# Optimization experiments

Measured on AMD Instinct MI355X. Metric: run time of the kernel, lower is better.

The kernel has to match this reference:

```python
import jax, jax.numpy as jnp
import numpy as np

B, S, D = 8, 1024, 1024
H, K = 16, 64  # num_heads, key_dim
NEG_INF = -1e9  # Keras _large_compatible_negative for float32


def setup_inputs() -> dict:
    key = jax.random.key(0)
    ks = jax.random.split(key, 10)
    x = jax.random.normal(ks[0], (B, S, D), dtype=jnp.float32)
    mask = jax.random.bernoulli(ks[1], 0.9, (B, S))  # bool per-token mask
    w = lambda k, shp: (0.02 * jax.random.normal(k, shp, dtype=jnp.float32))
    return {
        "input_tensor": x,
        "input_mask": mask,
        "Wq": w(ks[2], (D, H, K)), "bq": jnp.zeros((H, K), jnp.float32),
        "Wk": w(ks[3], (D, H, K)), "bk": jnp.zeros((H, K), jnp.float32),
        "Wv": w(ks[4], (D, H, K)), "bv": jnp.zeros((H, K), jnp.float32),
        "Wo": w(ks[5], (H, K, D)), "bo": jnp.zeros((D,), jnp.float32),
    }


def reference(input_tensor, input_mask, Wq, bq, Wk, bk, Wv, bv, Wo, bo):
    x = input_tensor
    # QKV projections: [B,S,D] x [D,H,K] -> [B,S,H,K]
    q = jnp.einsum("bsd,dhk->bshk", x, Wq) + bq
    k = jnp.einsum("bsd,dhk->bshk", x, Wk) + bk
    v = jnp.einsum("bsd,dhk->bshk", x, Wv) + bv
    # scaled dot-product scores: [B,H,Sq,Sk]
    scores = jnp.einsum("bqhk,bshk->bhqs", q, k) / jnp.sqrt(
        jnp.asarray(K, x.dtype))
    # mask = logical_and(mask[...,None], mask[...,None,:]) per example
    m2 = (input_mask[:, :, None] & input_mask[:, None, :])  # [B,Sq,Sk]
    scores = scores + (1.0 - m2[:, None, :, :].astype(x.dtype)) * NEG_INF
    probs = jax.nn.softmax(scores, axis=-1)
    # attend and project out: [B,S,H,K] -> [B,S,D]
    ctx = jnp.einsum("bhqs,bshk->bqhk", probs, v)
    return jnp.einsum("bqhk,hkd->bqd", ctx, Wo) + bo
```

## Files before the change

kernel.cpp:

```cpp
#include <hip/hip_runtime.h>
#include <math.h>

#define Ss 1024
#define Dd 1024
#define Hh 16
#define Kk 64

typedef __bf16 bf16x8 __attribute__((ext_vector_type(8)));
typedef __bf16 bf16x4 __attribute__((ext_vector_type(4)));
typedef float  f32x4  __attribute__((ext_vector_type(4)));

#define MFMA16(a, b, c) __builtin_amdgcn_mfma_f32_16x16x32_bf16(a, b, c, 0, 0, 0)

#define XB_E   8388608u
#define WT_E   3145728u
#define WOT_E  1048576u
#define QKV_E  8388608u

__global__ __launch_bounds__(256) void prep(
    const float* __restrict__ x,
    const float* __restrict__ Wq, const float* __restrict__ Wk,
    const float* __restrict__ Wv, const float* __restrict__ Wo,
    __bf16* __restrict__ xb, __bf16* __restrict__ WT, __bf16* __restrict__ WoT)
{
    __shared__ float tile[64][65];
    const int z = blockIdx.z;
    const int t = threadIdx.x;

    if (z == 4) {
        size_t blk = blockIdx.y * 16 + blockIdx.x;
        const float4* src = (const float4*)(x + blk * 32768);
        bf16x4* dst = (bf16x4*)(((__bf16*)xb) + blk * 32768);
        #pragma unroll
        for (int u = 0; u < 32; ++u) {
            float4 v = src[u * 256 + t];
            dst[u * 256 + t] =
                (bf16x4){(__bf16)v.x, (__bf16)v.y, (__bf16)v.z, (__bf16)v.w};
        }
        return;
    }

    const float* src = (z == 0) ? Wq : (z == 1) ? Wk : (z == 2) ? Wv : Wo;
    __bf16* dst = (z < 3) ? (WT + (size_t)z * 1048576) : WoT;

    int r0 = blockIdx.y * 64, c0 = blockIdx.x * 64;
    int rr = t >> 2, cg = (t & 3) * 16;

    #pragma unroll
    for (int u = 0; u < 4; ++u) {
        float4 v = *(const float4*)(src + (size_t)(r0 + rr) * 1024 + c0 + cg + u * 4);
        tile[rr][cg + u * 4 + 0] = v.x;
        tile[rr][cg + u * 4 + 1] = v.y;
        tile[rr][cg + u * 4 + 2] = v.z;
        tile[rr][cg + u * 4 + 3] = v.w;
    }
    __syncthreads();
    bf16x8 o0, o1;
    #pragma unroll
    for (int jj = 0; jj < 8; ++jj) o0[jj] = (__bf16)tile[cg + jj][rr];
    #pragma unroll
    for (int jj = 0; jj < 8; ++jj) o1[jj] = (__bf16)tile[cg + 8 + jj][rr];
    __bf16* dp = dst + (size_t)(c0 + rr) * 1024 + r0 + cg;
    *(bf16x8*)dp = o0;
    *(bf16x8*)(dp + 8) = o1;
}

__global__ __launch_bounds__(256) void gemm_bt(
    const __bf16* __restrict__ A, const __bf16* __restrict__ Bt, int mode,
    __bf16* __restrict__ qb, __bf16* __restrict__ kb, __bf16* __restrict__ vb,
    const float* __restrict__ bq, const float* __restrict__ bk,
    const float* __restrict__ bv,
    float* __restrict__ outf, const float* __restrict__ bo)
{
    __shared__ __align__(16) __bf16 As[2][128][32];
    __shared__ __align__(16) __bf16 Bs[2][128][32];

    const int t = threadIdx.x;
    const int wave = t >> 6, lane = t & 63;
    const int quad = lane >> 4, l16 = lane & 15;
    const int wm = wave >> 1, wn = wave & 1;
    const int m0 = blockIdx.y * 128, n0 = blockIdx.x * 128;

    const int sr = t >> 2;
    const int sc = (t & 3) * 8;

    f32x4 acc[4][4];
    #pragma unroll
    for (int i = 0; i < 4; ++i)
        #pragma unroll
        for (int j = 0; j < 4; ++j) acc[i][j] = (f32x4){0.f, 0.f, 0.f, 0.f};

    const __bf16* pa0 = A + (size_t)(m0 + sr) * 1024 + sc;
    const __bf16* pa1 = A + (size_t)(m0 + sr + 64) * 1024 + sc;
    const __bf16* pb0 = Bt + (size_t)(n0 + sr) * 1024 + sc;
    const __bf16* pb1 = Bt + (size_t)(n0 + sr + 64) * 1024 + sc;

    bf16x8 ra0 = *(const bf16x8*)(pa0);
    bf16x8 ra1 = *(const bf16x8*)(pa1);
    bf16x8 rb0 = *(const bf16x8*)(pb0);
    bf16x8 rb1 = *(const bf16x8*)(pb1);

    for (int k0 = 0; k0 < 1024; k0 += 32) {
        const int p = (k0 >> 5) & 1;
        *(bf16x8*)&As[p][sr][sc] = ra0;
        *(bf16x8*)&As[p][sr + 64][sc] = ra1;
        *(bf16x8*)&Bs[p][sr][sc] = rb0;
        *(bf16x8*)&Bs[p][sr + 64][sc] = rb1;
        __syncthreads();

        const int kn = k0 + 32;
        if (kn < 1024) {
            ra0 = *(const bf16x8*)(pa0 + kn);
            ra1 = *(const bf16x8*)(pa1 + kn);
            rb0 = *(const bf16x8*)(pb0 + kn);
            rb1 = *(const bf16x8*)(pb1 + kn);
        }

        bf16x8 af[4], bfr[4];
        #pragma unroll
        for (int i = 0; i < 4; ++i)
            af[i] = *(const bf16x8*)&As[p][wm * 64 + i * 16 + l16][quad * 8];
        #pragma unroll
        for (int j = 0; j < 4; ++j)
            bfr[j] = *(const bf16x8*)&Bs[p][wn * 64 + j * 16 + l16][quad * 8];
        #pragma unroll
        for (int i = 0; i < 4; ++i)
            #pragma unroll
            for (int j = 0; j < 4; ++j)
                acc[i][j] = MFMA16(af[i], bfr[j], acc[i][j]);
    }

    if (mode == 0) {
        const int z = n0 >> 10;
        const float* bias = (z == 0) ? bq : (z == 1) ? bk : bv;
        const float sc2 = (z == 0) ? 0.125f : 1.0f;
        #pragma unroll
        for (int i = 0; i < 4; ++i) {
            int row = m0 + wm * 64 + i * 16 + quad * 4;
            int b = row >> 10, s = row & 1023;
            #pragma unroll
            for (int j = 0; j < 4; ++j) {
                int n1 = (n0 + wn * 64 + j * 16 + l16) & 1023;
                int h = n1 >> 6, ch = n1 & 63;
                float bia = bias[n1];
                if (z < 2) {
                    __bf16* dst = ((z == 0) ? qb : kb)
                        + ((size_t)(b * Hh + h) * Ss + s) * Kk + ch;
                    #pragma unroll
                    for (int r = 0; r < 4; ++r)
                        dst[(size_t)r * Kk] = (__bf16)((acc[i][j][r] + bia) * sc2);
                } else {
                    bf16x4 o;
                    #pragma unroll
                    for (int r = 0; r < 4; ++r) o[r] = (__bf16)(acc[i][j][r] + bia);
                    *(bf16x4*)(vb + ((size_t)(b * Hh + h) * Kk + ch) * Ss + s) = o;
                }
            }
        }
    } else {
        #pragma unroll
        for (int i = 0; i < 4; ++i) {
            int row = m0 + wm * 64 + i * 16 + quad * 4;
            #pragma unroll
            for (int j = 0; j < 4; ++j) {
                int n = n0 + wn * 64 + j * 16 + l16;
                float bia = bo[n];
                #pragma unroll
                for (int r = 0; r < 4; ++r)
                    outf[(size_t)(row + r) * 1024 + n] = acc[i][j][r] + bia;
            }
        }
    }
}

__global__ __launch_bounds__(256) void attn(
    const __bf16* __restrict__ qb, const __bf16* __restrict__ kb,
    const __bf16* __restrict__ vb, const int* __restrict__ mask,
    __bf16* __restrict__ ctx)
{
    const int bh = blockIdx.x;
    const int q0 = blockIdx.y * 128;
    const int b  = bh >> 4;
    const int h  = bh & 15;
    const size_t base = (size_t)bh * Ss * Kk;

    __shared__ __align__(16) __bf16 Qs[128][72];
    __shared__ __align__(16) __bf16 Ks[64][72];
    __shared__ __align__(16) __bf16 VTs[64][72];
    __shared__ __align__(16) __bf16 Ps[4][32][72];
    __shared__ float mkf[1024];

    const int t    = threadIdx.x;
    const int wave = t >> 6, lane = t & 63;
    const int quad = lane >> 4, l16 = lane & 15;
    const int qbase = wave * 32;

    #pragma unroll
    for (int p = 0; p < 4; ++p) {
        int idx = t + p * 256;
        int r = idx >> 3, g = idx & 7;
        *(bf16x8*)&Qs[r][g * 8] =
            *(const bf16x8*)(qb + base + (size_t)(q0 + r) * Kk + g * 8);
    }
    {
        int4 mi = *(const int4*)(mask + b * Ss + t * 4);
        mkf[t * 4 + 0] = (float)mi.x;
        mkf[t * 4 + 1] = (float)mi.y;
        mkf[t * 4 + 2] = (float)mi.z;
        mkf[t * 4 + 3] = (float)mi.w;
    }

    const int r0 = t >> 3, c0 = (t & 7) * 8;
    bf16x8 kr0, kr1, vr0, vr1;
    kr0 = *(const bf16x8*)(kb + base + (size_t)(r0) * Kk + c0);
    kr1 = *(const bf16x8*)(kb + base + (size_t)(r0 + 32) * Kk + c0);
    vr0 = *(const bf16x8*)(vb + base + (size_t)(r0) * Ss + c0);
    vr1 = *(const bf16x8*)(vb + base + (size_t)(r0 + 32) * Ss + c0);

    __syncthreads();

    bf16x8 aq[2][2];
    #pragma unroll
    for (int rg = 0; rg < 2; ++rg) {
        aq[rg][0] = *(const bf16x8*)&Qs[qbase + rg * 16 + l16][quad * 8];
        aq[rg][1] = *(const bf16x8*)&Qs[qbase + rg * 16 + l16][32 + quad * 8];
    }
    float mqf[2][4], omqf[2][4];
    #pragma unroll
    for (int rg = 0; rg < 2; ++rg)
        #pragma unroll
        for (int i = 0; i < 4; ++i) {
            float m = mkf[q0 + qbase + rg * 16 + quad * 4 + i];
            mqf[rg][i] = m; omqf[rg][i] = 1.0f - m;
        }

    f32x4 O[2][4];
    float lsum[2][4];
    #pragma unroll
    for (int rg = 0; rg < 2; ++rg)
        #pragma unroll
        for (int nb = 0; nb < 4; ++nb) O[rg][nb] = (f32x4){0.f, 0.f, 0.f, 0.f};
    #pragma unroll
    for (int rg = 0; rg < 2; ++rg)
        #pragma unroll
        for (int i = 0; i < 4; ++i) lsum[rg][i] = 0.f;

    for (int kt = 0; kt < Ss; kt += 64) {
        __syncthreads();
        *(bf16x8*)&Ks[r0][c0] = kr0;
        *(bf16x8*)&Ks[r0 + 32][c0] = kr1;
        *(bf16x8*)&VTs[r0][c0] = vr0;
        *(bf16x8*)&VTs[r0 + 32][c0] = vr1;
        __syncthreads();

        int ktn = kt + 64;
        if (ktn < Ss) {
            kr0 = *(const bf16x8*)(kb + base + (size_t)(ktn + r0) * Kk + c0);
            kr1 = *(const bf16x8*)(kb + base + (size_t)(ktn + r0 + 32) * Kk + c0);
            vr0 = *(const bf16x8*)(vb + base + (size_t)(r0) * Ss + ktn + c0);
            vr1 = *(const bf16x8*)(vb + base + (size_t)(r0 + 32) * Ss + ktn + c0);
        }

        float mkv[4];
        #pragma unroll
        for (int nb = 0; nb < 4; ++nb) mkv[nb] = mkf[kt + nb * 16 + l16];

        bf16x8 kb0[4], kb1[4];
        #pragma unroll
        for (int nb = 0; nb < 4; ++nb) {
            kb0[nb] = *(const bf16x8*)&Ks[nb * 16 + l16][quad * 8];
            kb1[nb] = *(const bf16x8*)&Ks[nb * 16 + l16][32 + quad * 8];
        }

        f32x4 s[2][4];
        #pragma unroll
        for (int rg = 0; rg < 2; ++rg)
            #pragma unroll
            for (int nb = 0; nb < 4; ++nb) {
                f32x4 a = (f32x4){0.f, 0.f, 0.f, 0.f};
                a = MFMA16(aq[rg][0], kb0[nb], a);
                a = MFMA16(aq[rg][1], kb1[nb], a);
                s[rg][nb] = a;
            }

        #pragma unroll
        for (int rg = 0; rg < 2; ++rg)
            #pragma unroll
            for (int i = 0; i < 4; ++i) {
                float ls = 0.f;
                #pragma unroll
                for (int nb = 0; nb < 4; ++nb) {
                    float p = __expf(s[rg][nb][i]) * mkv[nb];
                    p = p * mqf[rg][i] + omqf[rg][i];
                    Ps[wave][rg * 16 + quad * 4 + i][nb * 16 + l16] = (__bf16)p;
                    ls += p;
                }
                lsum[rg][i] += ls;
            }

        bf16x8 ap0[2], ap1[2];
        #pragma unroll
        for (int rg = 0; rg < 2; ++rg) {
            ap0[rg] = *(const bf16x8*)&Ps[wave][rg * 16 + l16][quad * 8];
            ap1[rg] = *(const bf16x8*)&Ps[wave][rg * 16 + l16][32 + quad * 8];
        }
        #pragma unroll
        for (int nb = 0; nb < 4; ++nb) {
            bf16x8 vb0 = *(const bf16x8*)&VTs[nb * 16 + l16][quad * 8];
            bf16x8 vb1 = *(const bf16x8*)&VTs[nb * 16 + l16][32 + quad * 8];
            #pragma unroll
            for (int rg = 0; rg < 2; ++rg) {
                O[rg][nb] = MFMA16(ap0[rg], vb0, O[rg][nb]);
                O[rg][nb] = MFMA16(ap1[rg], vb1, O[rg][nb]);
            }
        }
    }

    #pragma unroll
    for (int rg = 0; rg < 2; ++rg)
        #pragma unroll
        for (int i = 0; i < 4; ++i) {
            float l = lsum[rg][i];
            l += __shfl_xor(l, 1);
            l += __shfl_xor(l, 2);
            l += __shfl_xor(l, 4);
            l += __shfl_xor(l, 8);
            float inv = 1.0f / l;
            int srow = q0 + qbase + rg * 16 + quad * 4 + i;
            __bf16* dst = ctx + ((size_t)(b * Ss + srow) * Hh + h) * Kk;
            #pragma unroll
            for (int nb = 0; nb < 4; ++nb)
                dst[nb * 16 + l16] = (__bf16)(O[rg][nb][i] * inv);
        }
}

extern "C" void kernel_launch(void* const* d_in, const int* in_sizes, int n_in,
                              void* d_out, int out_size, void* d_ws, size_t ws_size,
                              hipStream_t stream) {
    const float* x    = (const float*)d_in[0];
    const int*   mask = (const int*)d_in[1];
    const float* Wq   = (const float*)d_in[2];
    const float* bq   = (const float*)d_in[3];
    const float* Wk   = (const float*)d_in[4];
    const float* bk   = (const float*)d_in[5];
    const float* Wv   = (const float*)d_in[6];
    const float* bv   = (const float*)d_in[7];
    const float* Wo   = (const float*)d_in[8];
    const float* bo   = (const float*)d_in[9];

    __bf16* xb   = (__bf16*)d_ws;
    __bf16* WT   = xb + XB_E;
    __bf16* WoT  = WT + WT_E;
    __bf16* qb   = WoT + WOT_E;
    __bf16* kb   = qb + QKV_E;
    __bf16* vb   = kb + QKV_E;
    __bf16* ctxb = vb + QKV_E;
    float* out = (float*)d_out;

    prep<<<dim3(16, 16, 5), 256, 0, stream>>>(x, Wq, Wk, Wv, Wo, xb, WT, WoT);
    gemm_bt<<<dim3(24, 64), 256, 0, stream>>>(xb, WT, 0, qb, kb, vb,
                                              bq, bk, bv, nullptr, nullptr);
    attn<<<dim3(128, 8), 256, 0, stream>>>(qb, kb, vb, mask, ctxb);
    gemm_bt<<<dim3(8, 64), 256, 0, stream>>>(ctxb, WoT, 1, nullptr, nullptr,
                                             nullptr, nullptr, nullptr, nullptr,
                                             out, bo);
}
```

Measured before the change: 271.7 us.

## Fuse x bf16 conversion into QKV GEMM and vectorize epilogue stores

```diff
diff --git a/kernel.cpp b/kernel.cpp
--- a/kernel.cpp
+++ b/kernel.cpp
@@ -12,33 +12,23 @@
 
 #define MFMA16(a, b, c) __builtin_amdgcn_mfma_f32_16x16x32_bf16(a, b, c, 0, 0, 0)
 
-#define XB_E   8388608u
 #define WT_E   3145728u
 #define WOT_E  1048576u
 #define QKV_E  8388608u
 
+__device__ __forceinline__ bf16x8 pack8(float4 a, float4 b) {
+    return (bf16x8){(__bf16)a.x, (__bf16)a.y, (__bf16)a.z, (__bf16)a.w,
+                    (__bf16)b.x, (__bf16)b.y, (__bf16)b.z, (__bf16)b.w};
+}
+
 __global__ __launch_bounds__(256) void prep(
-    const float* __restrict__ x,
     const float* __restrict__ Wq, const float* __restrict__ Wk,
     const float* __restrict__ Wv, const float* __restrict__ Wo,
-    __bf16* __restrict__ xb, __bf16* __restrict__ WT, __bf16* __restrict__ WoT)
+    __bf16* __restrict__ WT, __bf16* __restrict__ WoT)
 {
     __shared__ float tile[64][65];
     const int z = blockIdx.z;
     const int t = threadIdx.x;
-
-    if (z == 4) {
-        size_t blk = blockIdx.y * 16 + blockIdx.x;
-        const float4* src = (const float4*)(x + blk * 32768);
-        bf16x4* dst = (bf16x4*)(((__bf16*)xb) + blk * 32768);
-        #pragma unroll
-        for (int u = 0; u < 32; ++u) {
-            float4 v = src[u * 256 + t];
-            dst[u * 256 + t] =
-                (bf16x4){(__bf16)v.x, (__bf16)v.y, (__bf16)v.z, (__bf16)v.w};
-        }
-        return;
-    }
 
     const float* src = (z == 0) ? Wq : (z == 1) ? Wk : (z == 2) ? Wv : Wo;
     __bf16* dst = (z < 3) ? (WT + (size_t)z * 1048576) : WoT;
@@ -66,7 +56,7 @@
 }
 
 __global__ __launch_bounds__(256) void gemm_bt(
-    const __bf16* __restrict__ A, const __bf16* __restrict__ Bt, int mode,
+    const void* __restrict__ Av, const __bf16* __restrict__ Bt, int mode,
     __bf16* __restrict__ qb, __bf16* __restrict__ kb, __bf16* __restrict__ vb,
     const float* __restrict__ bq, const float* __restrict__ bk,
     const float* __restrict__ bv,
@@ -84,34 +74,60 @@
     const int sr = t >> 2;
     const int sc = (t & 3) * 8;
 
+    const int z = (mode == 0) ? (n0 >> 10) : 3;
+    const bool swp = (z != 2);
+
     f32x4 acc[4][4];
     #pragma unroll
     for (int i = 0; i < 4; ++i)
         #pragma unroll
         for (int j = 0; j < 4; ++j) acc[i][j] = (f32x4){0.f, 0.f, 0.f, 0.f};
 
-    const __bf16* pa0 = A + (size_t)(m0 + sr) * 1024 + sc;
-    const __bf16* pa1 = A + (size_t)(m0 + sr + 64) * 1024 + sc;
+    const float*  Af = (const float*)Av;
+    const __bf16* Ab = (const __bf16*)Av;
     const __bf16* pb0 = Bt + (size_t)(n0 + sr) * 1024 + sc;
     const __bf16* pb1 = Bt + (size_t)(n0 + sr + 64) * 1024 + sc;
 
-    bf16x8 ra0 = *(const bf16x8*)(pa0);
-    bf16x8 ra1 = *(const bf16x8*)(pa1);
-    bf16x8 rb0 = *(const bf16x8*)(pb0);
-    bf16x8 rb1 = *(const bf16x8*)(pb1);
+    float4 fa0a, fa0b, fa1a, fa1b;
+    bf16x8 ra0, ra1;
+    bf16x8 rb0, rb1;
+
+    if (mode == 0) {
+        const float* p0 = Af + (size_t)(m0 + sr) * 1024 + sc;
+        const float* p1 = Af + (size_t)(m0 + sr + 64) * 1024 + sc;
+        fa0a = *(const float4*)(p0);     fa0b = *(const float4*)(p0 + 4);
+        fa1a = *(const float4*)(p1);     fa1b = *(const float4*)(p1 + 4);
+    } else {
+        ra0 = *(const bf16x8*)(Ab + (size_t)(m0 + sr) * 1024 + sc);
+        ra1 = *(const bf16x8*)(Ab + (size_t)(m0 + sr + 64) * 1024 + sc);
+    }
+    rb0 = *(const bf16x8*)(pb0);
+    rb1 = *(const bf16x8*)(pb1);
 
     for (int k0 = 0; k0 < 1024; k0 += 32) {
         const int p = (k0 >> 5) & 1;
-        *(bf16x8*)&As[p][sr][sc] = ra0;
-        *(bf16x8*)&As[p][sr + 64][sc] = ra1;
+        if (mode == 0) {
+            *(bf16x8*)&As[p][sr][sc] = pack8(fa0a, fa0b);
+            *(bf16x8*)&As[p][sr + 64][sc] = pack8(fa1a, fa1b);
+        } else {
+            *(bf16x8*)&As[p][sr][sc] = ra0;
+            *(bf16x8*)&As[p][sr + 64][sc] = ra1;
+        }
         *(bf16x8*)&Bs[p][sr][sc] = rb0;
         *(bf16x8*)&Bs[p][sr + 64][sc] = rb1;
         __syncthreads();
 
         const int kn = k0 + 32;
         if (kn < 1024) {
-            ra0 = *(const bf16x8*)(pa0 + kn);
-            ra1 = *(const bf16x8*)(pa1 + kn);
+            if (mode == 0) {
+                const float* p0 = Af + (size_t)(m0 + sr) * 1024 + kn + sc;
+                const float* p1 = Af + (size_t)(m0 + sr + 64) * 1024 + kn + sc;
+                fa0a = *(const float4*)(p0);     fa0b = *(const float4*)(p0 + 4);
+                fa1a = *(const float4*)(p1);     fa1b = *(const float4*)(p1 + 4);
+            } else {
+                ra0 = *(const bf16x8*)(Ab + (size_t)(m0 + sr) * 1024 + kn + sc);
+                ra1 = *(const bf16x8*)(Ab + (size_t)(m0 + sr + 64) * 1024 + kn + sc);
+            }
             rb0 = *(const bf16x8*)(pb0 + kn);
             rb1 = *(const bf16x8*)(pb1 + kn);
         }
@@ -123,33 +139,54 @@
         #pragma unroll
         for (int j = 0; j < 4; ++j)
             bfr[j] = *(const bf16x8*)&Bs[p][wn * 64 + j * 16 + l16][quad * 8];
-        #pragma unroll
-        for (int i = 0; i < 4; ++i)
-            #pragma unroll
-            for (int j = 0; j < 4; ++j)
-                acc[i][j] = MFMA16(af[i], bfr[j], acc[i][j]);
+        if (swp) {
+            #pragma unroll
+            for (int i = 0; i < 4; ++i)
+                #pragma unroll
+                for (int j = 0; j < 4; ++j)
+                    acc[i][j] = MFMA16(bfr[j], af[i], acc[i][j]);
+        } else {
+            #pragma unroll
+            for (int i = 0; i < 4; ++i)
+                #pragma unroll
+                for (int j = 0; j < 4; ++j)
+                    acc[i][j] = MFMA16(af[i], bfr[j], acc[i][j]);
+        }
     }
 
     if (mode == 0) {
-        const int z = n0 >> 10;
         const float* bias = (z == 0) ? bq : (z == 1) ? bk : bv;
-        const float sc2 = (z == 0) ? 0.125f : 1.0f;
-        #pragma unroll
-        for (int i = 0; i < 4; ++i) {
-            int row = m0 + wm * 64 + i * 16 + quad * 4;
-            int b = row >> 10, s = row & 1023;
-            #pragma unroll
-            for (int j = 0; j < 4; ++j) {
-                int n1 = (n0 + wn * 64 + j * 16 + l16) & 1023;
-                int h = n1 >> 6, ch = n1 & 63;
-                float bia = bias[n1];
-                if (z < 2) {
-                    __bf16* dst = ((z == 0) ? qb : kb)
-                        + ((size_t)(b * Hh + h) * Ss + s) * Kk + ch;
-                    #pragma unroll
-                    for (int r = 0; r < 4; ++r)
-                        dst[(size_t)r * Kk] = (__bf16)((acc[i][j][r] + bia) * sc2);
-                } else {
+        if (z < 2) {
+            __bf16* dst0 = (z == 0) ? qb : kb;
+            const float sc2 = (z == 0) ? 0.125f : 1.0f;
+            const int h = ((n0 & 1023) >> 6) + wn;
+            #pragma unroll
+            for (int i = 0; i < 4; ++i) {
+                int m = m0 + wm * 64 + i * 16 + l16;
+                int b = m >> 10, s = m & 1023;
+                __bf16* dst = dst0 + ((size_t)(b * Hh + h) * Ss + s) * Kk;
+                #pragma unroll
+                for (int j = 0; j < 4; ++j) {
+                    int ch0 = j * 16 + quad * 4;
+                    float4 b4 = *(const float4*)(bias + (n0 & 1023) + wn * 64 + ch0);
+                    bf16x4 o;
+                    o[0] = (__bf16)((acc[i][j][0] + b4.x) * sc2);
+                    o[1] = (__bf16)((acc[i][j][1] + b4.y) * sc2);
+                    o[2] = (__bf16)((acc[i][j][2] + b4.z) * sc2);
+                    o[3] = (__bf16)((acc[i][j][3] + b4.w) * sc2);
+                    *(bf16x4*)(dst + ch0) = o;
+                }
+            }
+        } else {
+            #pragma unroll
+            for (int i = 0; i < 4; ++i) {
+                int row = m0 + wm * 64 + i * 16 + quad * 4;
+                int b = row >> 10, s = row & 1023;
+                #pragma unroll
+                for (int j = 0; j < 4; ++j) {
+                    int n1 = (n0 + wn * 64 + j * 16 + l16) & 1023;
+                    int h = n1 >> 6, ch = n1 & 63;
+                    float bia = bv[n1];
                     bf16x4 o;
                     #pragma unroll
                     for (int r = 0; r < 4; ++r) o[r] = (__bf16)(acc[i][j][r] + bia);
@@ -160,14 +197,17 @@
     } else {
         #pragma unroll
         for (int i = 0; i < 4; ++i) {
-            int row = m0 + wm * 64 + i * 16 + quad * 4;
+            int m = m0 + wm * 64 + i * 16 + l16;
             #pragma unroll
             for (int j = 0; j < 4; ++j) {
-                int n = n0 + wn * 64 + j * 16 + l16;
-                float bia = bo[n];
-                #pragma unroll
-                for (int r = 0; r < 4; ++r)
-                    outf[(size_t)(row + r) * 1024 + n] = acc[i][j][r] + bia;
+                int n = n0 + wn * 64 + j * 16 + quad * 4;
+                float4 b4 = *(const float4*)(bo + n);
+                float4 o;
+                o.x = acc[i][j][0] + b4.x;
+                o.y = acc[i][j][1] + b4.y;
+                o.z = acc[i][j][2] + b4.z;
+                o.w = acc[i][j][3] + b4.w;
+                *(float4*)(outf + (size_t)m * 1024 + n) = o;
             }
         }
     }
@@ -184,30 +224,23 @@
     const int h  = bh & 15;
     const size_t base = (size_t)bh * Ss * Kk;
 
-    __shared__ __align__(16) __bf16 Qs[128][72];
     __shared__ __align__(16) __bf16 Ks[64][72];
     __shared__ __align__(16) __bf16 VTs[64][72];
     __shared__ __align__(16) __bf16 Ps[4][32][72];
-    __shared__ float mkf[1024];
+    __shared__ __bf16 mkb[1024];
+    __shared__ float  lds_l[4][32];
 
     const int t    = threadIdx.x;
     const int wave = t >> 6, lane = t & 63;
     const int quad = lane >> 4, l16 = lane & 15;
     const int qbase = wave * 32;
 
-    #pragma unroll
-    for (int p = 0; p < 4; ++p) {
-        int idx = t + p * 256;
-        int r = idx >> 3, g = idx & 7;
-        *(bf16x8*)&Qs[r][g * 8] =
-            *(const bf16x8*)(qb + base + (size_t)(q0 + r) * Kk + g * 8);
-    }
     {
         int4 mi = *(const int4*)(mask + b * Ss + t * 4);
-        mkf[t * 4 + 0] = (float)mi.x;
-        mkf[t * 4 + 1] = (float)mi.y;
-        mkf[t * 4 + 2] = (float)mi.z;
-        mkf[t * 4 + 3] = (float)mi.w;
+        mkb[t * 4 + 0] = (__bf16)(float)mi.x;
+        mkb[t * 4 + 1] = (__bf16)(float)mi.y;
+        mkb[t * 4 + 2] = (__bf16)(float)mi.z;
+        mkb[t * 4 + 3] = (__bf16)(float)mi.w;
     }
 
     const int r0 = t >> 3, c0 = (t & 7) * 8;
@@ -217,20 +250,22 @@
     vr0 = *(const bf16x8*)(vb + base + (size_t)(r0) * Ss + c0);
     vr1 = *(const bf16x8*)(vb + base + (size_t)(r0 + 32) * Ss + c0);
 
+    bf16x8 aq[2][2];
+    #pragma unroll
+    for (int rg = 0; rg < 2; ++rg) {
+        const __bf16* qr = qb + base + (size_t)(q0 + qbase + rg * 16 + l16) * Kk;
+        aq[rg][0] = *(const bf16x8*)(qr + quad * 8);
+        aq[rg][1] = *(const bf16x8*)(qr + 32 + quad * 8);
+    }
+
     __syncthreads();
 
-    bf16x8 aq[2][2];
-    #pragma unroll
-    for (int rg = 0; rg < 2; ++rg) {
-        aq[rg][0] = *(const bf16x8*)&Qs[qbase + rg * 16 + l16][quad * 8];
-        aq[rg][1] = *(const bf16x8*)&Qs[qbase + rg * 16 + l16][32 + quad * 8];
-    }
     float mqf[2][4], omqf[2][4];
     #pragma unroll
     for (int rg = 0; rg < 2; ++rg)
         #pragma unroll
         for (int i = 0; i < 4; ++i) {
-            float m = mkf[q0 + qbase + rg * 16 + quad * 4 + i];
+            float m = (float)mkb[q0 + qbase + rg * 16 + quad * 4 + i];
             mqf[rg][i] = m; omqf[rg][i] = 1.0f - m;
         }
 
@@ -263,7 +298,7 @@
 
         float mkv[4];
         #pragma unroll
-        for (int nb = 0; nb < 4; ++nb) mkv[nb] = mkf[kt + nb * 16 + l16];
+        for (int nb = 0; nb < 4; ++nb) mkv[nb] = (float)mkb[kt + nb * 16 + l16];
 
         bf16x8 kb0[4], kb1[4];
         #pragma unroll
@@ -310,8 +345,8 @@
             bf16x8 vb1 = *(const bf16x8*)&VTs[nb * 16 + l16][32 + quad * 8];
             #pragma unroll
             for (int rg = 0; rg < 2; ++rg) {
-                O[rg][nb] = MFMA16(ap0[rg], vb0, O[rg][nb]);
-                O[rg][nb] = MFMA16(ap1[rg], vb1, O[rg][nb]);
+                O[rg][nb] = MFMA16(vb0, ap0[rg], O[rg][nb]);
+                O[rg][nb] = MFMA16(vb1, ap1[rg], O[rg][nb]);
             }
         }
     }
@@ -325,13 +360,26 @@
             l += __shfl_xor(l, 2);
             l += __shfl_xor(l, 4);
             l += __shfl_xor(l, 8);
-            float inv = 1.0f / l;
-            int srow = q0 + qbase + rg * 16 + quad * 4 + i;
-            __bf16* dst = ctx + ((size_t)(b * Ss + srow) * Hh + h) * Kk;
-            #pragma unroll
-            for (int nb = 0; nb < 4; ++nb)
-                dst[nb * 16 + l16] = (__bf16)(O[rg][nb][i] * inv);
-        }
+            if (l16 == 0) lds_l[wave][rg * 16 + quad * 4 + i] = l;
+        }
+    float invl[2];
+    #pragma unroll
+    for (int rg = 0; rg < 2; ++rg) invl[rg] = 1.0f / lds_l[wave][rg * 16 + l16];
+
+    #pragma unroll
+    for (int rg = 0; rg < 2; ++rg) {
+        int q = q0 + qbase + rg * 16 + l16;
+        __bf16* dst = ctx + ((size_t)(b * Ss + q) * Hh + h) * Kk;
+        #pragma unroll
+        for (int nb = 0; nb < 4; ++nb) {
+            bf16x4 o;
+            o[0] = (__bf16)(O[rg][nb][0] * invl[rg]);
+            o[1] = (__bf16)(O[rg][nb][1] * invl[rg]);
+            o[2] = (__bf16)(O[rg][nb][2] * invl[rg]);
+            o[3] = (__bf16)(O[rg][nb][3] * invl[rg]);
+            *(bf16x4*)(dst + nb * 16 + quad * 4) = o;
+        }
+    }
 }
 
 extern "C" void kernel_launch(void* const* d_in, const int* in_sizes, int n_in,
@@ -348,8 +396,7 @@
     const float* Wo   = (const float*)d_in[8];
     const float* bo   = (const float*)d_in[9];
 
-    __bf16* xb   = (__bf16*)d_ws;
-    __bf16* WT   = xb + XB_E;
+    __bf16* WT   = (__bf16*)d_ws;
     __bf16* WoT  = WT + WT_E;
     __bf16* qb   = WoT + WOT_E;
     __bf16* kb   = qb + QKV_E;
@@ -357,8 +404,8 @@
     __bf16* ctxb = vb + QKV_E;
     float* out = (float*)d_out;
 
-    prep<<<dim3(16, 16, 5), 256, 0, stream>>>(x, Wq, Wk, Wv, Wo, xb, WT, WoT);
-    gemm_bt<<<dim3(24, 64), 256, 0, stream>>>(xb, WT, 0, qb, kb, vb,
+    prep<<<dim3(16, 16, 4), 256, 0, stream>>>(Wq, Wk, Wv, Wo, WT, WoT);
+    gemm_bt<<<dim3(24, 64), 256, 0, stream>>>(x, WT, 0, qb, kb, vb,
                                               bq, bk, bv, nullptr, nullptr);
     attn<<<dim3(128, 8), 256, 0, stream>>>(qb, kb, vb, mask, ctxb);
     gemm_bt<<<dim3(8, 64), 256, 0, stream>>>(ctxb, WoT, 1, nullptr, nullptr,
```

Measured after the change: 436.6 us. 1.61x slower.
